# Kernel tuning notes

Hardware: AMD Instinct MI355X
Metric: run time of the kernel (lower is better)

## Reference

```python
import jax, jax.numpy as jnp
import numpy as np
from jax.ops import segment_sum

N_NODES = 100000


def gcn_conv(x, edge_index, W, b, n_nodes):
    # PyG GCNConv: add self-loops, symmetric normalization, linear, scatter-add, bias
    src = jnp.concatenate([edge_index[0], jnp.arange(n_nodes, dtype=edge_index.dtype)])
    dst = jnp.concatenate([edge_index[1], jnp.arange(n_nodes, dtype=edge_index.dtype)])
    deg = segment_sum(jnp.ones(src.shape[0], dtype=x.dtype), dst, num_segments=n_nodes)
    dinv = jnp.where(deg > 0, jax.lax.rsqrt(deg), 0.0)
    norm = dinv[src] * dinv[dst]            # [E+N]
    h = x @ W                               # [N, out] dense GEMM first (PyG order)
    msg = h[src] * norm[:, None]            # gather + scale, [E+N, out]
    out = segment_sum(msg, dst, num_segments=n_nodes)  # scatter-add
    return out + b


def setup_inputs() -> dict:
    key = jax.random.key(0)
    k1, k2, k3, k4, k5, k6 = jax.random.split(key, 6)
    in_c, hid_c, out_c = 128, 128, 64
    n_edges = 1600000
    x = jax.random.normal(k1, (N_NODES, in_c), dtype=jnp.float32)
    edge_index = jax.random.randint(k2, (2, n_edges), 0, N_NODES, dtype=jnp.int64)
    # Glorot-ish init for weights, zeros for bias (PyG defaults)
    W1 = jax.random.normal(k3, (in_c, hid_c), dtype=jnp.float32) / np.sqrt(in_c)
    b1 = jnp.zeros((hid_c,), dtype=jnp.float32)
    W2 = jax.random.normal(k4, (hid_c, out_c), dtype=jnp.float32) / np.sqrt(hid_c)
    b2 = jnp.zeros((out_c,), dtype=jnp.float32)
    return {"x": x, "edge_index": edge_index, "W1": W1, "b1": b1, "W2": W2, "b2": b2}


def reference(x, edge_index, W1, b1, W2, b2):
    h = gcn_conv(x, edge_index, W1, b1, N_NODES)
    h = jax.nn.relu(h)
    out = gcn_conv(h, edge_index, W2, b2, N_NODES)
    return out
```

## Files before the change

### kernel.cpp

```cpp
#include <hip/hip_runtime.h>
#include <hip/hip_fp16.h>

#define NN 100000
#define NBKT 196
#define BCAP 16384

using f16x8 = __attribute__((ext_vector_type(8))) _Float16;
using f32x4 = __attribute__((ext_vector_type(4))) float;

__device__ __forceinline__ void fma4(float4& a, float s, const float4& w) {
  a.x = fmaf(s, w.x, a.x);
  a.y = fmaf(s, w.y, a.y);
  a.z = fmaf(s, w.z, a.z);
  a.w = fmaf(s, w.w, a.w);
}

__device__ __forceinline__ void add8(float* a, uint4 q) {
  const __half2* p = (const __half2*)&q;
#pragma unroll
  for (int j = 0; j < 4; ++j) {
    float2 f = __half22float2(p[j]);
    a[2 * j]     += f.x;
    a[2 * j + 1] += f.y;
  }
}

__device__ __forceinline__ unsigned packh2(float x, float y) {
  __half2 h = __floats2half2_rn(x, y);
  return *(unsigned*)&h;
}

__global__ __launch_bounds__(256) void k_prep(const float* __restrict__ W1,
                                              const float* __restrict__ W2,
                                              _Float16* __restrict__ wt1,
                                              _Float16* __restrict__ wt2,
                                              int* __restrict__ gcur,
                                              const int* __restrict__ e,
                                              int* __restrict__ flag, int E) {
  const int b = blockIdx.x;
  const int tid = threadIdx.x;
  if (b < 64) {
    int i = b * 256 + tid;
    int n = i >> 7, k = i & 127;
    wt1[i] = (_Float16)W1[k * 128 + n];
  } else if (b < 96) {
    int i = (b - 64) * 256 + tid;
    int n = i >> 7, k = i & 127;
    wt2[i] = (_Float16)W2[k * 64 + n];
  } else {
    if (tid < NBKT) gcur[tid] = tid * BCAP;
    if (tid == 255) {
      int n = E < 64 ? E : 64;
      int m = 1;
      for (int i = 0; i < n; ++i)
        if (e[2 * i + 1] != 0) { m = 0; break; }
      *flag = m;
    }
  }
}

__global__ __launch_bounds__(256) void k_binA(const int* __restrict__ e,
                                              const int* __restrict__ flag,
                                              int* __restrict__ gcur,
                                              unsigned int* __restrict__ tmp, int E) {
  __shared__ int cnt[256];
  __shared__ int pcur[256];
  const int tid = threadIdx.x;
  const int start = blockIdx.x * 4096;
  const int m = *flag;
  cnt[tid] = 0;
  __syncthreads();
  int ss[16], dd[16];
#pragma unroll
  for (int k = 0; k < 16; ++k) {
    int i = start + tid + k * 256;
    int s = -1, d = 0;
    if (i < E) {
      if (m) {
        s = (int)((const long long*)e)[i];
        d = (int)((const long long*)e)[E + i];
      } else {
        s = e[i];
        d = e[E + i];
      }
      atomicAdd(&cnt[d >> 9], 1);
    }
    ss[k] = s; dd[k] = d;
  }
  __syncthreads();
  if (tid < NBKT && cnt[tid] > 0) pcur[tid] = atomicAdd(&gcur[tid], cnt[tid]);
  __syncthreads();
#pragma unroll
  for (int k = 0; k < 16; ++k) {
    if (ss[k] >= 0) {
      int b = dd[k] >> 9;
      int p = atomicAdd(&pcur[b], 1);
      tmp[p] = ((unsigned)ss[k] << 9) | (unsigned)(dd[k] & 511);
    }
  }
}

__global__ __launch_bounds__(256) void k_bkt_scan(const int* __restrict__ gcur,
                                                  int* __restrict__ bktbase,
                                                  int* __restrict__ rowptr) {
  __shared__ int s[256];
  const int tid = threadIdx.x;
  int v = (tid < NBKT) ? (gcur[tid] - tid * BCAP) : 0;
  s[tid] = v;
  __syncthreads();
#pragma unroll
  for (int off = 1; off < 256; off <<= 1) {
    int t = (tid >= off) ? s[tid - off] : 0;
    __syncthreads();
    s[tid] += t;
    __syncthreads();
  }
  if (tid < NBKT) bktbase[tid] = s[tid] - v;
  if (tid == 255) {
    bktbase[NBKT] = s[255];
    rowptr[NN] = s[255];
  }
}

__global__ __launch_bounds__(256) void k_binB(const unsigned int* __restrict__ tmp,
                                              const int* __restrict__ gcur,
                                              const int* __restrict__ bktbase,
                                              int* __restrict__ rowptr,
                                              float* __restrict__ dinv,
                                              int* __restrict__ srcs) {
  __shared__ int hist[512];
  __shared__ int lofs[512];
  __shared__ int sbuf[256];
  const int b = blockIdx.x;
  const int tid = threadIdx.x;
  const int tbeg = b * BCAP;
  const int tend = gcur[b];
  const int base = bktbase[b];
  hist[tid] = 0;
  hist[tid + 256] = 0;
  __syncthreads();
  for (int j = tbeg + tid; j < tend; j += 256) atomicAdd(&hist[tmp[j] & 511], 1);
  __syncthreads();
  int a0 = hist[2 * tid], a1 = hist[2 * tid + 1];
  int sv = a0 + a1;
  sbuf[tid] = sv;
  __syncthreads();
#pragma unroll
  for (int off = 1; off < 256; off <<= 1) {
    int t = (tid >= off) ? sbuf[tid - off] : 0;
    __syncthreads();
    sbuf[tid] += t;
    __syncthreads();
  }
  int excl = sbuf[tid] - sv;
  lofs[2 * tid] = excl;
  lofs[2 * tid + 1] = excl + a0;
  __syncthreads();
  for (int i = tid; i < 512; i += 256) {
    int node = (b << 9) + i;
    if (node < NN) {
      rowptr[node] = base + lofs[i];
      dinv[node] = rsqrtf((float)(hist[i] + 1));
    }
  }
  __syncthreads();
  for (int j = tbeg + tid; j < tend; j += 256) {
    unsigned v = tmp[j];
    int p = base + atomicAdd(&lofs[v & 511], 1);
    srcs[p] = (int)(v >> 9);
  }
}

template <int N, bool AHALF>
__global__ __launch_bounds__(256) void k_gemm_mfma(const void* __restrict__ Av,
                                                   const _Float16* __restrict__ Wt,
                                                   const float* __restrict__ dinv,
                                                   _Float16* __restrict__ out, int M) {
  constexpr int NF = N / 16;
  __shared__ _Float16 As[64 * 136];
  __shared__ _Float16 Bs[N * 136];
  const int tid = threadIdx.x;
  const long long row0 = (long long)blockIdx.x * 64;
  if (AHALF) {
    const _Float16* A = (const _Float16*)Av;
#pragma unroll
    for (int t = 0; t < 4; ++t) {
      int i = tid + t * 256;
      int m = i >> 4, q = i & 15;
      long long row = row0 + m;
      uint4 v = make_uint4(0, 0, 0, 0);
      if (row < M) v = ((const uint4*)A)[row * 16 + q];
      *(uint4*)&As[m * 136 + q * 8] = v;
    }
  } else {
    const float* A = (const float*)Av;
#pragma unroll
    for (int t = 0; t < 8; ++t) {
      int i = tid + t * 256;
      int m = i >> 5, q = i & 31;
      long long row = row0 + m;
      float4 v = make_float4(0.f, 0.f, 0.f, 0.f);
      if (row < M) v = ((const float4*)A)[row * 32 + q];
      uint2 w2 = make_uint2(packh2(v.x, v.y), packh2(v.z, v.w));
      *(uint2*)&As[m * 136 + q * 4] = w2;
    }
  }
#pragma unroll
  for (int t = 0; t < N / 16; ++t) {
    int i = tid + t * 256;
    int n = i >> 4, q = i & 15;
    uint4 v = ((const uint4*)Wt)[i];
    *(uint4*)&Bs[n * 136 + q * 8] = v;
  }
  __syncthreads();
  const int lane = tid & 63;
  const int wrow = (tid >> 6) * 16;
  const int r = lane & 15, g = lane >> 4;
  f32x4 acc[NF] = {};
#pragma unroll
  for (int ks = 0; ks < 4; ++ks) {
    f16x8 av = *(const f16x8*)&As[(wrow + r) * 136 + ks * 32 + g * 8];
#pragma unroll
    for (int cf = 0; cf < NF; ++cf) {
      f16x8 bv = *(const f16x8*)&Bs[(cf * 16 + r) * 136 + ks * 32 + g * 8];
      acc[cf] = __builtin_amdgcn_mfma_f32_16x16x32_f16(av, bv, acc[cf], 0, 0, 0);
    }
  }
#pragma unroll
  for (int q = 0; q < 4; ++q) {
    long long row = row0 + wrow + g * 4 + q;
    if (row < M) {
      float sc = dinv[row];
#pragma unroll
      for (int cf = 0; cf < NF; ++cf)
        out[row * N + cf * 16 + r] = (_Float16)(sc * acc[cf][q]);
    }
  }
}

template <int C, bool RELU16>
__global__ __launch_bounds__(256) void k_gather_s(const int* __restrict__ rowptr,
                                                  const int* __restrict__ srcs,
                                                  const float* __restrict__ dinv,
                                                  const _Float16* __restrict__ h,
                                                  const float* __restrict__ b,
                                                  void* __restrict__ outv) {
  constexpr int LPN = C / 8;
  constexpr int NPW = 64 / LPN;
  constexpr int NPB = NPW * 4;
  const int wave = threadIdx.x >> 6;
  const int lane = threadIdx.x & 63;
  const int grp = lane / LPN;
  const int li = lane % LPN;
  const int node = blockIdx.x * NPB + wave * NPW + grp;
  if (node >= NN) return;
  const float dd = dinv[node];
  float acc[8];
  {
    uint4 q = *(const uint4*)(h + (long long)node * C + li * 8);
    const __half2* p = (const __half2*)&q;
#pragma unroll
    for (int j = 0; j < 4; ++j) {
      float2 f = __half22float2(p[j]);
      acc[2 * j]     = f.x;
      acc[2 * j + 1] = f.y;
    }
  }
  const int beg = rowptr[node], end = rowptr[node + 1];
  int e = beg;
  for (; e + 4 <= end; e += 4) {
    int s0 = srcs[e], s1 = srcs[e + 1], s2 = srcs[e + 2], s3 = srcs[e + 3];
    uint4 q0 = *(const uint4*)(h + (long long)s0 * C + li * 8);
    uint4 q1 = *(const uint4*)(h + (long long)s1 * C + li * 8);
    uint4 q2 = *(const uint4*)(h + (long long)s2 * C + li * 8);
    uint4 q3 = *(const uint4*)(h + (long long)s3 * C + li * 8);
    add8(acc, q0);
    add8(acc, q1);
    add8(acc, q2);
    add8(acc, q3);
  }
  for (; e < end; ++e) {
    uint4 q0 = *(const uint4*)(h + (long long)srcs[e] * C + li * 8);
    add8(acc, q0);
  }
  const float4* b4 = (const float4*)b;
  float4 bb0 = b4[li * 2], bb1 = b4[li * 2 + 1];
  float o[8];
  o[0] = fmaf(dd, acc[0], bb0.x);
  o[1] = fmaf(dd, acc[1], bb0.y);
  o[2] = fmaf(dd, acc[2], bb0.z);
  o[3] = fmaf(dd, acc[3], bb0.w);
  o[4] = fmaf(dd, acc[4], bb1.x);
  o[5] = fmaf(dd, acc[5], bb1.y);
  o[6] = fmaf(dd, acc[6], bb1.z);
  o[7] = fmaf(dd, acc[7], bb1.w);
  if (RELU16) {
#pragma unroll
    for (int j = 0; j < 8; ++j) o[j] = fmaxf(o[j], 0.f);
    uint4 w;
    w.x = packh2(o[0], o[1]);
    w.y = packh2(o[2], o[3]);
    w.z = packh2(o[4], o[5]);
    w.w = packh2(o[6], o[7]);
    *(uint4*)((_Float16*)outv + (long long)node * C + li * 8) = w;
  } else {
    float4* op = (float4*)((float*)outv + (long long)node * C + li * 8);
    op[0] = make_float4(o[0], o[1], o[2], o[3]);
    op[1] = make_float4(o[4], o[5], o[6], o[7]);
  }
}

__global__ void k_zero_i32(int* p, int n) {
  int i = blockIdx.x * 256 + threadIdx.x;
  if (i < n) p[i] = 0;
}

__global__ void k_detect_f(const int* __restrict__ e, int* flag, int E) {
  if (threadIdx.x == 0 && blockIdx.x == 0) {
    int n = E < 64 ? E : 64;
    int m = 1;
    for (int i = 0; i < n; ++i)
      if (e[2 * i + 1] != 0) { m = 0; break; }
    *flag = m;
  }
}

__global__ void k_deg_count(const int* __restrict__ e, const int* __restrict__ flag,
                            int* __restrict__ deg, int E) {
  int i = blockIdx.x * 256 + threadIdx.x;
  if (i >= E) return;
  int m = *flag;
  int d = m ? e[2 * (E + i)] : e[E + i];
  atomicAdd(&deg[d], 1);
}

__global__ void k_dinv_f(const int* __restrict__ deg, float* __restrict__ dinv) {
  int i = blockIdx.x * 256 + threadIdx.x;
  if (i < NN) dinv[i] = rsqrtf((float)(deg[i] + 1));
}

template <int N, bool RELU>
__global__ __launch_bounds__(256) void k_gemm_v(const float* __restrict__ A,
                                                const float* __restrict__ W,
                                                float* __restrict__ out, int M) {
  constexpr int K4 = 32;
  constexpr int N4 = N / 4;
  constexpr int CG = N4;
  constexpr int ROWS = (256 / CG) * 4;
  __shared__ float4 Wl[128 * N4];
  __shared__ float4 Xl[ROWS * K4];
  const int tid = threadIdx.x;
  const float4* W4 = (const float4*)W;
  for (int i = tid; i < 128 * N4; i += 256) Wl[i] = W4[i];
  const long long row0 = (long long)blockIdx.x * ROWS;
  const float4* A4 = (const float4*)A;
  for (int i = tid; i < ROWS * K4; i += 256) {
    int r = i >> 5;
    long long row = row0 + r;
    float4 v = make_float4(0.f, 0.f, 0.f, 0.f);
    if (row < M) v = A4[row * K4 + (i & 31)];
    if (RELU) {
      v.x = fmaxf(v.x, 0.f); v.y = fmaxf(v.y, 0.f);
      v.z = fmaxf(v.z, 0.f); v.w = fmaxf(v.w, 0.f);
    }
    Xl[i] = v;
  }
  __syncthreads();
  const int c = tid % CG;
  const int rb = (tid / CG) * 4;
  float4 a0 = make_float4(0, 0, 0, 0), a1 = a0, a2 = a0, a3 = a0;
#pragma unroll 4
  for (int k4 = 0; k4 < K4; ++k4) {
    float4 w0 = Wl[(k4 * 4 + 0) * N4 + c];
    float4 w1 = Wl[(k4 * 4 + 1) * N4 + c];
    float4 w2 = Wl[(k4 * 4 + 2) * N4 + c];
    float4 w3 = Wl[(k4 * 4 + 3) * N4 + c];
    float4 x0 = Xl[(rb + 0) * K4 + k4];
    float4 x1 = Xl[(rb + 1) * K4 + k4];
    float4 x2 = Xl[(rb + 2) * K4 + k4];
    float4 x3 = Xl[(rb + 3) * K4 + k4];
    fma4(a0, x0.x, w0); fma4(a0, x0.y, w1); fma4(a0, x0.z, w2); fma4(a0, x0.w, w3);
    fma4(a1, x1.x, w0); fma4(a1, x1.y, w1); fma4(a1, x1.z, w2); fma4(a1, x1.w, w3);
    fma4(a2, x2.x, w0); fma4(a2, x2.y, w1); fma4(a2, x2.z, w2); fma4(a2, x2.w, w3);
    fma4(a3, x3.x, w0); fma4(a3, x3.y, w1); fma4(a3, x3.z, w2); fma4(a3, x3.w, w3);
  }
  float4* O4 = (float4*)out;
  long long row = row0 + rb;
  if (row + 0 < M) O4[(row + 0) * N4 + c] = a0;
  if (row + 1 < M) O4[(row + 1) * N4 + c] = a1;
  if (row + 2 < M) O4[(row + 2) * N4 + c] = a2;
  if (row + 3 < M) O4[(row + 3) * N4 + c] = a3;
}

template <int C>
__global__ void k_self_bias(const float* __restrict__ h, const float* __restrict__ dinv,
                            const float* __restrict__ b, float* __restrict__ out) {
  constexpr int C4 = C / 4;
  int gid = blockIdx.x * 256 + threadIdx.x;
  if (gid >= NN * C4) return;
  int node = gid / C4;
  int cq = gid % C4;
  float di = dinv[node];
  float sc = di * di;
  float4 v = ((const float4*)h)[gid];
  float4 bb = ((const float4*)b)[cq];
  float4 o;
  o.x = fmaf(v.x, sc, bb.x);
  o.y = fmaf(v.y, sc, bb.y);
  o.z = fmaf(v.z, sc, bb.z);
  o.w = fmaf(v.w, sc, bb.w);
  ((float4*)out)[gid] = o;
}

template <int C>
__global__ void k_scatter(const int* __restrict__ e, const int* __restrict__ flag,
                          const float* __restrict__ dinv, const float* __restrict__ h,
                          float* __restrict__ out, int E) {
  constexpr int TPE = C / 4;
  long long gid = (long long)blockIdx.x * blockDim.x + threadIdx.x;
  int ei = (int)(gid / TPE);
  int cq = (int)(gid % TPE);
  if (ei >= E) return;
  int m = *flag;
  int s, d;
  if (m) { s = e[2 * ei]; d = e[2 * (E + ei)]; }
  else   { s = e[ei];     d = e[E + ei]; }
  float nrm = dinv[s] * dinv[d];
  float4 v = ((const float4*)h)[(long long)s * TPE + cq];
  float* op = out + (long long)d * C + (long long)cq * 4;
  unsafeAtomicAdd(op + 0, v.x * nrm);
  unsafeAtomicAdd(op + 1, v.y * nrm);
  unsafeAtomicAdd(op + 2, v.z * nrm);
  unsafeAtomicAdd(op + 3, v.w * nrm);
}

extern "C" void kernel_launch(void* const* d_in, const int* in_sizes, int n_in,
                              void* d_out, int out_size, void* d_ws, size_t ws_size,
                              hipStream_t stream) {
  const float* x  = (const float*)d_in[0];
  const int*   e  = (const int*)d_in[1];
  const float* W1 = (const float*)d_in[2];
  const float* b1 = (const float*)d_in[3];
  const float* W2 = (const float*)d_in[4];
  const float* b2 = (const float*)d_in[5];
  float* out = (float*)d_out;
  const int E = in_sizes[1] / 2;

  char* ws = (char*)d_ws;
  const size_t o_flag    = 0;
  const size_t o_dinv    = 16;
  const size_t o_rowptr  = 400016;
  const size_t o_gcur    = 800032;
  const size_t o_bktbase = 800832;
  const size_t o_tmp     = 801632;
  const size_t o_srcs    = 13646688;
  const size_t o_wt1     = 20046688;
  const size_t o_wt2     = 20079456;
  const size_t o_h       = 20095840;
  const size_t o_out1    = 45695840;
  const size_t need_csr  = 71295840;

  int*      flag    = (int*)(ws + o_flag);
  float*    dinv    = (float*)(ws + o_dinv);
  int*      rowptr  = (int*)(ws + o_rowptr);
  int*      gcur    = (int*)(ws + o_gcur);
  int*      bktbase = (int*)(ws + o_bktbase);
  unsigned* tmp     = (unsigned*)(ws + o_tmp);
  int*      srcs    = (int*)(ws + o_srcs);
  _Float16* wt1     = (_Float16*)(ws + o_wt1);
  _Float16* wt2     = (_Float16*)(ws + o_wt2);
  _Float16* hh      = (_Float16*)(ws + o_h);
  _Float16* out1    = (_Float16*)(ws + o_out1);

  if (ws_size >= need_csr) {
    k_prep<<<97, 256, 0, stream>>>(W1, W2, wt1, wt2, gcur, e, flag, E);
    k_binA<<<(E + 4095) / 4096, 256, 0, stream>>>(e, flag, gcur, tmp, E);
    k_bkt_scan<<<1, 256, 0, stream>>>(gcur, bktbase, rowptr);
    k_binB<<<NBKT, 256, 0, stream>>>(tmp, gcur, bktbase, rowptr, dinv, srcs);

    k_gemm_mfma<128, false><<<(NN + 63) / 64, 256, 0, stream>>>(x, wt1, dinv, hh, NN);
    k_gather_s<128, true><<<(NN + 15) / 16, 256, 0, stream>>>(rowptr, srcs, dinv, hh, b1, out1);

    k_gemm_mfma<64, true><<<(NN + 63) / 64, 256, 0, stream>>>(out1, wt2, dinv, hh, NN);
    k_gather_s<64, false><<<(NN + 31) / 32, 256, 0, stream>>>(rowptr, srcs, dinv, hh, b2, out);
  } else {
    int*   deg   = (int*)(ws + 400016);
    float* hF    = (float*)(ws + (1 << 20));
    float* out1F = (float*)(ws + (1 << 20) + 51200000);
    k_detect_f<<<1, 64, 0, stream>>>(e, flag, E);
    k_zero_i32<<<(NN + 255) / 256, 256, 0, stream>>>(deg, NN);
    k_deg_count<<<(E + 255) / 256, 256, 0, stream>>>(e, flag, deg, E);
    k_dinv_f<<<(NN + 255) / 256, 256, 0, stream>>>(deg, dinv);
    k_gemm_v<128, false><<<(NN + 31) / 32, 256, 0, stream>>>(x, W1, hF, NN);
    k_self_bias<128><<<(NN * 32 + 255) / 256, 256, 0, stream>>>(hF, dinv, b1, out1F);
    long long tot1 = (long long)E * 32;
    k_scatter<128><<<(int)((tot1 + 255) / 256), 256, 0, stream>>>(e, flag, dinv, hF, out1F, E);
    k_gemm_v<64, true><<<(NN + 63) / 64, 256, 0, stream>>>(out1F, W2, hF, NN);
    k_self_bias<64><<<(NN * 16 + 255) / 256, 256, 0, stream>>>(hF, dinv, b2, out);
    long long tot2 = (long long)E * 16;
    k_scatter<64><<<(int)((tot2 + 255) / 256), 256, 0, stream>>>(e, flag, dinv, hF, out, E);
  }
}
```

Baseline: 224.2 us.

## Fuse weight prep and bucket scan into binning kernels, vectorize edge loads

Merges the weight transpose/convert and int64 detection into the first binning kernel, folds the single-block bucket scan into each binB block (every block redoes the 196-entry scan), and replaces the gcur init with a memset of zero-based counters. Edge index loads are widened to int4/int2 so each thread handles two edges per iteration. The aim is to cut two kernel launches and their serialization bubbles, and to improve load efficiency in the binning pass. The cost is redundant per-block scan work and an extra memset node.

After: 222.7 us. About the same (-0.7%).

```diff
diff --git a/kernel.cpp b/kernel.cpp
--- a/kernel.cpp
+++ b/kernel.cpp
@@ -30,120 +30,105 @@
   return *(unsigned*)&h;
 }
 
-__global__ __launch_bounds__(256) void k_prep(const float* __restrict__ W1,
+__global__ __launch_bounds__(256) void k_binA(const int* __restrict__ e,
+                                              const float* __restrict__ W1,
                                               const float* __restrict__ W2,
                                               _Float16* __restrict__ wt1,
                                               _Float16* __restrict__ wt2,
                                               int* __restrict__ gcur,
-                                              const int* __restrict__ e,
-                                              int* __restrict__ flag, int E) {
+                                              unsigned int* __restrict__ tmp,
+                                              int E, int nA) {
   const int b = blockIdx.x;
   const int tid = threadIdx.x;
-  if (b < 64) {
-    int i = b * 256 + tid;
-    int n = i >> 7, k = i & 127;
-    wt1[i] = (_Float16)W1[k * 128 + n];
-  } else if (b < 96) {
-    int i = (b - 64) * 256 + tid;
-    int n = i >> 7, k = i & 127;
-    wt2[i] = (_Float16)W2[k * 64 + n];
-  } else {
-    if (tid < NBKT) gcur[tid] = tid * BCAP;
-    if (tid == 255) {
-      int n = E < 64 ? E : 64;
-      int m = 1;
-      for (int i = 0; i < n; ++i)
-        if (e[2 * i + 1] != 0) { m = 0; break; }
-      *flag = m;
-    }
-  }
-}
-
-__global__ __launch_bounds__(256) void k_binA(const int* __restrict__ e,
-                                              const int* __restrict__ flag,
-                                              int* __restrict__ gcur,
-                                              unsigned int* __restrict__ tmp, int E) {
+  if (b >= nA) {
+    int wb = b - nA;
+    if (wb < 64) {
+      int i = wb * 256 + tid;
+      int n = i >> 7, k = i & 127;
+      wt1[i] = (_Float16)W1[k * 128 + n];
+    } else {
+      int i = (wb - 64) * 256 + tid;
+      int n = i >> 7, k = i & 127;
+      wt2[i] = (_Float16)W2[k * 64 + n];
+    }
+    return;
+  }
   __shared__ int cnt[256];
   __shared__ int pcur[256];
-  const int tid = threadIdx.x;
-  const int start = blockIdx.x * 4096;
-  const int m = *flag;
+  __shared__ int sm_flag;
   cnt[tid] = 0;
-  __syncthreads();
+  if (tid < 64) {
+    int n64 = E < 64 ? E : 64;
+    int odd = (tid < n64) ? e[2 * tid + 1] : 0;
+    unsigned long long nz = __ballot(odd != 0);
+    if (tid == 0) sm_flag = (nz == 0ull) ? 1 : 0;
+  }
+  __syncthreads();
+  const int m = sm_flag;
+  const bool pok = ((E & 1) == 0);
+  const int start = b * 4096;
   int ss[16], dd[16];
 #pragma unroll
-  for (int k = 0; k < 16; ++k) {
-    int i = start + tid + k * 256;
-    int s = -1, d = 0;
+  for (int k = 0; k < 8; ++k) {
+    int i = start + 2 * (tid + k * 256);
+    int s0 = -1, s1 = -1, d0 = 0, d1 = 0;
     if (i < E) {
       if (m) {
-        s = (int)((const long long*)e)[i];
-        d = (int)((const long long*)e)[E + i];
+        if (pok) {
+          int4 sp = ((const int4*)e)[i >> 1];
+          int4 dp = ((const int4*)e)[(E + i) >> 1];
+          s0 = sp.x; s1 = sp.z; d0 = dp.x; d1 = dp.z;
+        } else {
+          s0 = (int)((const long long*)e)[i];
+          d0 = (int)((const long long*)e)[E + i];
+          if (i + 1 < E) {
+            s1 = (int)((const long long*)e)[i + 1];
+            d1 = (int)((const long long*)e)[E + i + 1];
+          }
+        }
       } else {
-        s = e[i];
-        d = e[E + i];
+        if (pok) {
+          int2 sp = ((const int2*)e)[i >> 1];
+          int2 dp = ((const int2*)(e + E))[i >> 1];
+          s0 = sp.x; s1 = sp.y; d0 = dp.x; d1 = dp.y;
+        } else {
+          s0 = e[i]; d0 = e[E + i];
+          if (i + 1 < E) { s1 = e[i + 1]; d1 = e[E + i + 1]; }
+        }
       }
-      atomicAdd(&cnt[d >> 9], 1);
-    }
-    ss[k] = s; dd[k] = d;
-  }
-  __syncthreads();
-  if (tid < NBKT && cnt[tid] > 0) pcur[tid] = atomicAdd(&gcur[tid], cnt[tid]);
+      if (i + 1 >= E) s1 = -1;
+      atomicAdd(&cnt[d0 >> 9], 1);
+      if (s1 >= 0) atomicAdd(&cnt[d1 >> 9], 1);
+    }
+    ss[2 * k] = s0; dd[2 * k] = d0;
+    ss[2 * k + 1] = s1; dd[2 * k + 1] = d1;
+  }
+  __syncthreads();
+  if (tid < NBKT && cnt[tid] > 0)
+    pcur[tid] = tid * BCAP + atomicAdd(&gcur[tid], cnt[tid]);
   __syncthreads();
 #pragma unroll
   for (int k = 0; k < 16; ++k) {
     if (ss[k] >= 0) {
-      int b = dd[k] >> 9;
-      int p = atomicAdd(&pcur[b], 1);
+      int bk = dd[k] >> 9;
+      int p = atomicAdd(&pcur[bk], 1);
       tmp[p] = ((unsigned)ss[k] << 9) | (unsigned)(dd[k] & 511);
     }
-  }
-}
-
-__global__ __launch_bounds__(256) void k_bkt_scan(const int* __restrict__ gcur,
-                                                  int* __restrict__ bktbase,
-                                                  int* __restrict__ rowptr) {
-  __shared__ int s[256];
-  const int tid = threadIdx.x;
-  int v = (tid < NBKT) ? (gcur[tid] - tid * BCAP) : 0;
-  s[tid] = v;
-  __syncthreads();
-#pragma unroll
-  for (int off = 1; off < 256; off <<= 1) {
-    int t = (tid >= off) ? s[tid - off] : 0;
-    __syncthreads();
-    s[tid] += t;
-    __syncthreads();
-  }
-  if (tid < NBKT) bktbase[tid] = s[tid] - v;
-  if (tid == 255) {
-    bktbase[NBKT] = s[255];
-    rowptr[NN] = s[255];
   }
 }
 
 __global__ __launch_bounds__(256) void k_binB(const unsigned int* __restrict__ tmp,
                                               const int* __restrict__ gcur,
-                                              const int* __restrict__ bktbase,
                                               int* __restrict__ rowptr,
                                               float* __restrict__ dinv,
                                               int* __restrict__ srcs) {
+  __shared__ int sbuf[256];
   __shared__ int hist[512];
   __shared__ int lofs[512];
-  __shared__ int sbuf[256];
   const int b = blockIdx.x;
   const int tid = threadIdx.x;
-  const int tbeg = b * BCAP;
-  const int tend = gcur[b];
-  const int base = bktbase[b];
-  hist[tid] = 0;
-  hist[tid + 256] = 0;
-  __syncthreads();
-  for (int j = tbeg + tid; j < tend; j += 256) atomicAdd(&hist[tmp[j] & 511], 1);
-  __syncthreads();
-  int a0 = hist[2 * tid], a1 = hist[2 * tid + 1];
-  int sv = a0 + a1;
-  sbuf[tid] = sv;
+  int c = (tid < NBKT) ? gcur[tid] : 0;
+  sbuf[tid] = c;
   __syncthreads();
 #pragma unroll
   for (int off = 1; off < 256; off <<= 1) {
@@ -152,6 +137,30 @@
     sbuf[tid] += t;
     __syncthreads();
   }
+  const int total = sbuf[255];
+  const int incl = sbuf[b];
+  const int base_b = (b > 0) ? sbuf[b - 1] : 0;
+  const int cntb = incl - base_b;
+  if (b == 0 && tid == 0) rowptr[NN] = total;
+  __syncthreads();
+  hist[tid] = 0;
+  hist[tid + 256] = 0;
+  __syncthreads();
+  const int tbeg = b * BCAP;
+  const int tend = tbeg + cntb;
+  for (int j = tbeg + tid; j < tend; j += 256) atomicAdd(&hist[tmp[j] & 511], 1);
+  __syncthreads();
+  int a0 = hist[2 * tid], a1 = hist[2 * tid + 1];
+  int sv = a0 + a1;
+  sbuf[tid] = sv;
+  __syncthreads();
+#pragma unroll
+  for (int off = 1; off < 256; off <<= 1) {
+    int t = (tid >= off) ? sbuf[tid - off] : 0;
+    __syncthreads();
+    sbuf[tid] += t;
+    __syncthreads();
+  }
   int excl = sbuf[tid] - sv;
   lofs[2 * tid] = excl;
   lofs[2 * tid + 1] = excl + a0;
@@ -159,14 +168,14 @@
   for (int i = tid; i < 512; i += 256) {
     int node = (b << 9) + i;
     if (node < NN) {
-      rowptr[node] = base + lofs[i];
+      rowptr[node] = base_b + lofs[i];
       dinv[node] = rsqrtf((float)(hist[i] + 1));
     }
   }
   __syncthreads();
   for (int j = tbeg + tid; j < tend; j += 256) {
     unsigned v = tmp[j];
-    int p = base + atomicAdd(&lofs[v & 511], 1);
+    int p = base_b + atomicAdd(&lofs[v & 511], 1);
     srcs[p] = (int)(v >> 9);
   }
 }
@@ -451,32 +460,30 @@
   const size_t o_dinv    = 16;
   const size_t o_rowptr  = 400016;
   const size_t o_gcur    = 800032;
-  const size_t o_bktbase = 800832;
-  const size_t o_tmp     = 801632;
-  const size_t o_srcs    = 13646688;
-  const size_t o_wt1     = 20046688;
-  const size_t o_wt2     = 20079456;
-  const size_t o_h       = 20095840;
-  const size_t o_out1    = 45695840;
-  const size_t need_csr  = 71295840;
-
-  int*      flag    = (int*)(ws + o_flag);
-  float*    dinv    = (float*)(ws + o_dinv);
-  int*      rowptr  = (int*)(ws + o_rowptr);
-  int*      gcur    = (int*)(ws + o_gcur);
-  int*      bktbase = (int*)(ws + o_bktbase);
-  unsigned* tmp     = (unsigned*)(ws + o_tmp);
-  int*      srcs    = (int*)(ws + o_srcs);
-  _Float16* wt1     = (_Float16*)(ws + o_wt1);
-  _Float16* wt2     = (_Float16*)(ws + o_wt2);
-  _Float16* hh      = (_Float16*)(ws + o_h);
-  _Float16* out1    = (_Float16*)(ws + o_out1);
+  const size_t o_tmp     = 800832;
+  const size_t o_srcs    = 13645888;
+  const size_t o_wt1     = 20045888;
+  const size_t o_wt2     = 20078656;
+  const size_t o_h       = 20095040;
+  const size_t o_out1    = 45695040;
+  const size_t need_csr  = 71295040;
+
+  int*      flag   = (int*)(ws + o_flag);
+  float*    dinv   = (float*)(ws + o_dinv);
+  int*      rowptr = (int*)(ws + o_rowptr);
+  int*      gcur   = (int*)(ws + o_gcur);
+  unsigned* tmp    = (unsigned*)(ws + o_tmp);
+  int*      srcs   = (int*)(ws + o_srcs);
+  _Float16* wt1    = (_Float16*)(ws + o_wt1);
+  _Float16* wt2    = (_Float16*)(ws + o_wt2);
+  _Float16* hh     = (_Float16*)(ws + o_h);
+  _Float16* out1   = (_Float16*)(ws + o_out1);
 
   if (ws_size >= need_csr) {
-    k_prep<<<97, 256, 0, stream>>>(W1, W2, wt1, wt2, gcur, e, flag, E);
-    k_binA<<<(E + 4095) / 4096, 256, 0, stream>>>(e, flag, gcur, tmp, E);
-    k_bkt_scan<<<1, 256, 0, stream>>>(gcur, bktbase, rowptr);
-    k_binB<<<NBKT, 256, 0, stream>>>(tmp, gcur, bktbase, rowptr, dinv, srcs);
+    const int nA = (E + 4095) / 4096;
+    hipMemsetAsync(gcur, 0, NBKT * sizeof(int), stream);
+    k_binA<<<nA + 96, 256, 0, stream>>>(e, W1, W2, wt1, wt2, gcur, tmp, E, nA);
+    k_binB<<<NBKT, 256, 0, stream>>>(tmp, gcur, rowptr, dinv, srcs);
 
     k_gemm_mfma<128, false><<<(NN + 63) / 64, 256, 0, stream>>>(x, wt1, dinv, hh, NN);
     k_gather_s<128, true><<<(NN + 15) / 16, 256, 0, stream>>>(rowptr, srcs, dinv, hh, b1, out1);
```
